# Kernel tuning notes

Hardware: AMD Instinct MI355X
Metric: run time of the kernel (lower is better)

## Reference

```python
import jax, jax.numpy as jnp
import numpy as np
from jax import lax

B, C_IN, T = 64, 16, 8192
HID, OUT = 64, 10
NEW_T = T // 4            # two MaxPool1d(2)
N_NODES = B * NEW_T       # 131072
N_EDGES = 2_097_152       # avg degree 16


def setup_inputs() -> dict:
    key = jax.random.key(0)
    ks = jax.random.split(key, 8)
    x = jax.random.normal(ks[0], (B, C_IN, T), dtype=jnp.float32)
    edge_index = jax.random.randint(ks[1], (2, N_EDGES), 0, N_NODES, dtype=jnp.int32)
    s = 0.05
    return {
        "x": x,
        "edge_index": edge_index,
        "conv1_w": jax.random.normal(ks[2], (16, C_IN, 5), dtype=jnp.float32) * s,
        "conv1_b": jnp.zeros((16,), jnp.float32),
        "conv2_w": jax.random.normal(ks[3], (32, 16, 5), dtype=jnp.float32) * s,
        "conv2_b": jnp.zeros((32,), jnp.float32),
        "gcn1_w": jax.random.normal(ks[4], (32, HID), dtype=jnp.float32) * s,
        "gcn1_b": jnp.zeros((HID,), jnp.float32),
        "gcn2_w": jax.random.normal(ks[5], (HID, HID), dtype=jnp.float32) * s,
        "gcn2_b": jnp.zeros((HID,), jnp.float32),
        "cls_w": jax.random.normal(ks[6], (HID, OUT), dtype=jnp.float32) * s,
        "cls_b": jnp.zeros((OUT,), jnp.float32),
    }


def conv1d(x, w, b):
    # x: [B, Cin, T], w: [Cout, Cin, K], padding=2 -> same length
    y = lax.conv_general_dilated(x, w, window_strides=(1,), padding=[(2, 2)],
                                 dimension_numbers=("NCH", "OIH", "NCH"))
    return y + b[None, :, None]


def maxpool2(x):
    # non-overlapping MaxPool1d(kernel=2) over last dim
    b, c, t = x.shape
    return x.reshape(b, c, t // 2, 2).max(axis=-1)


def gcn_conv(x, edge_index, W, b, n):
    # PyG GCNConv: add self-loops, symmetric normalization, scatter-add aggregate
    row, col = edge_index[0], edge_index[1]   # source j, target i
    loop = jnp.arange(n, dtype=row.dtype)
    row = jnp.concatenate([row, loop])
    col = jnp.concatenate([col, loop])
    deg = jax.ops.segment_sum(jnp.ones(row.shape, x.dtype), col, num_segments=n)
    dis = jnp.where(deg > 0, lax.rsqrt(deg), jnp.zeros_like(deg))
    norm = dis[row] * dis[col]                # [E+N]
    xw = x @ W                                # [N, out]
    msg = xw[row] * norm[:, None]             # gather along edges
    out = jax.ops.segment_sum(msg, col, num_segments=n)
    return out + b


def reference(x, edge_index, conv1_w, conv1_b, conv2_w, conv2_b,
              gcn1_w, gcn1_b, gcn2_w, gcn2_b, cls_w, cls_b):
    h = maxpool2(jax.nn.relu(conv1d(x, conv1_w, conv1_b)))     # [B,16,T/2]
    h = maxpool2(jax.nn.relu(conv1d(h, conv2_w, conv2_b)))     # [B,32,T/4]
    feat = h.transpose(0, 2, 1).reshape(-1, 32)                # [B*new_T, 32]
    n = feat.shape[0]
    g = jax.nn.relu(gcn_conv(feat, edge_index, gcn1_w, gcn1_b, n))
    g = jax.nn.relu(gcn_conv(g, edge_index, gcn2_w, gcn2_b, n))
    pooled = g.reshape(B, -1, HID).mean(axis=1)                # [B, HID]
    return pooled @ cls_w + cls_b                               # [B, OUT]
```

## Files before the change

### kernel.cpp

```cpp
#include <hip/hip_runtime.h>
#include <hip/hip_bf16.h>
#include <hip/hip_fp16.h>

#define BATCH 64
#define C_IN 16
#define T0 8192
#define T1 4096
#define T2 2048
#define N_NODES (BATCH * T2)
#define HID 64
#define NOUT 10

#define NCB 256
#define CB_SHIFT 9
#define CB_TGT 512
#define RCAP 9216
#define PC_EDGES 2048
#define PC_CAP 28

#define PK_RMASK 0x1FFFF

#define EC 1024

#define ZROW N_NODES

#define ROWW 24

#define FP8_SCALE 256.0f
#define FP8_SINV  (1.0f / 256.0f)

typedef __fp16 half8 __attribute__((ext_vector_type(8)));
typedef __fp16 half4v __attribute__((ext_vector_type(4)));
typedef float floatx4 __attribute__((ext_vector_type(4)));
typedef float floatx2 __attribute__((ext_vector_type(2)));

__global__ __launch_bounds__(256) void conv1_partition(
    const float* __restrict__ x, const float* __restrict__ w,
    const float* __restrict__ bias, __fp16* __restrict__ h1,
    const int* __restrict__ ei, int E,
    int* __restrict__ rcnt, int* __restrict__ gpairs,
    float* __restrict__ pool, unsigned char* __restrict__ xw,
    unsigned char* __restrict__ xw2) {
  __shared__ int smem_i[NCB + NCB * PC_CAP];
  if ((blockIdx.x & 1) == 0) {
    __fp16* xs = (__fp16*)smem_i;
    int bid = blockIdx.x >> 1;
    int b = bid >> 4;
    int tp0 = (bid & 15) * 256;
    if (bid == 0) {
      for (int k = threadIdx.x; k < BATCH * HID; k += 256) pool[k] = 0.f;
      if (threadIdx.x < 16) {
        ((unsigned*)(xw + (size_t)ZROW * 64))[threadIdx.x] = 0u;
        ((unsigned*)(xw2 + (size_t)ZROW * 64))[threadIdx.x] = 0u;
      }
    }
    int t_base = 2 * tp0 - 8;
    const float* xb = x + (size_t)b * C_IN * T0;
    for (int idx = threadIdx.x; idx < 16 * 132; idx += 256) {
      int ci = idx & 15;
      int c4 = idx >> 4;
      int gt = t_base + c4 * 4;
      float4 v = make_float4(0.f, 0.f, 0.f, 0.f);
      if (gt >= 0 && gt + 4 <= T0) v = *(const float4*)(xb + ci * T0 + gt);
      __fp16* d = xs + (c4 * 4) * ROWW + ci;
      d[0] = (__fp16)v.x;
      d[ROWW] = (__fp16)v.y;
      d[2 * ROWW] = (__fp16)v.z;
      d[3 * ROWW] = (__fp16)v.w;
    }
    int ln = threadIdx.x & 15;
    int q = (threadIdx.x & 63) >> 4;
    int wib = threadIdx.x >> 6;
    half8 wb[3];
#pragma unroll
    for (int ks = 0; ks < 3; ++ks) {
      int kk = ks * 2 + (q >> 1);
#pragma unroll
      for (int j = 0; j < 8; ++j) {
        int ci = (q & 1) * 8 + j;
        float wv = (kk < 5) ? w[(ln * 16 + ci) * 5 + kk] : 0.f;
        wb[ks][j] = (__fp16)wv;
      }
    }
    float bv = bias[ln];
    __syncthreads();
    int qh = q >> 1, qo = (q & 1) * 8;
#pragma unroll 2
    for (int mtl = 0; mtl < 8; ++mtl) {
      int mt = wib * 8 + mtl;
      int posb = mt * 16 + ln + qh + 6;
      half8 a0 = *(const half8*)(xs + posb * ROWW + qo);
      half8 a1 = *(const half8*)(xs + (posb + 2) * ROWW + qo);
      half8 a2 = *(const half8*)(xs + (posb + 4) * ROWW + qo);
      floatx4 c0 = {0.f, 0.f, 0.f, 0.f};
      c0 = __builtin_amdgcn_mfma_f32_16x16x32_f16(a0, wb[0], c0, 0, 0, 0);
      c0 = __builtin_amdgcn_mfma_f32_16x16x32_f16(a1, wb[1], c0, 0, 0, 0);
      c0 = __builtin_amdgcn_mfma_f32_16x16x32_f16(a2, wb[2], c0, 0, 0, 0);
      int tp = tp0 + mt * 8 + q * 2;
      size_t o = ((size_t)b * T1 + tp) * 16 + ln;
      h1[o] = (__fp16)fmaxf(fmaxf(c0[0], c0[1]) + bv, 0.f);
      h1[o + 16] = (__fp16)fmaxf(fmaxf(c0[2], c0[3]) + bv, 0.f);
    }
  } else {
    int* lcnt = smem_i;
    int* lpk = smem_i + NCB;
    int pid = blockIdx.x >> 1;
    if (threadIdx.x < NCB) lcnt[threadIdx.x] = 0;
    __syncthreads();
    int e0 = pid * PC_EDGES;
#pragma unroll
    for (int j = 0; j < PC_EDGES / 256; ++j) {
      int e = e0 + j * 256 + threadIdx.x;
      if (e < E) {
        int r = ei[e];
        int c = ei[E + e];
        int cb = c >> CB_SHIFT;
        int pk = r | ((c & (CB_TGT - 1)) << 17);
        int slot = atomicAdd(&lcnt[cb], 1);
        if (slot < PC_CAP) {
          lpk[cb * PC_CAP + slot] = pk;
        } else {
          int pos = atomicAdd(&rcnt[cb], 1);
          if (pos < RCAP) gpairs[(size_t)cb * RCAP + pos] = pk;
        }
      }
    }
    __syncthreads();
    int t = threadIdx.x;
    if (t < NCB) {
      int n = lcnt[t];
      if (n > PC_CAP) n = PC_CAP;
      if (n > 0) {
        int base = atomicAdd(&rcnt[t], n);
        int* dst = gpairs + (size_t)t * RCAP;
        for (int k = 0; k < n; ++k) {
          int p = base + k;
          if (p < RCAP) dst[p] = lpk[t * PC_CAP + k];
        }
      }
    }
  }
}

__global__ __launch_bounds__(256) void conv2_gemm1(const __fp16* __restrict__ h1,
    const float* __restrict__ w, const float* __restrict__ bias,
    const float* __restrict__ W1, const float* __restrict__ dis,
    unsigned char* __restrict__ xw) {
  __shared__ __fp16 xs[520 * ROWW];
  __shared__ __fp16 fs[256 * 40];
  int b = blockIdx.x >> 3;
  int tp0 = (blockIdx.x & 7) * 256;
  int t_base = 2 * tp0 - 2;
  for (int idx = threadIdx.x; idx < 520 * 2; idx += 256) {
    int row = idx >> 1;
    int hf = idx & 1;
    int gt = t_base + row;
    half8 v;
#pragma unroll
    for (int j = 0; j < 8; ++j) v[j] = (__fp16)0.f;
    if (gt >= 0 && gt < T1) v = *(const half8*)(h1 + ((size_t)b * T1 + gt) * 16 + hf * 8);
    *(half8*)(xs + row * ROWW + hf * 8) = v;
  }
  int ln = threadIdx.x & 15;
  int q = (threadIdx.x & 63) >> 4;
  int wib = threadIdx.x >> 6;
  half8 wb[2][3];
#pragma unroll
  for (int nt = 0; nt < 2; ++nt)
#pragma unroll
    for (int ks = 0; ks < 3; ++ks) {
      int kk = ks * 2 + (q >> 1);
#pragma unroll
      for (int j = 0; j < 8; ++j) {
        int ci = (q & 1) * 8 + j;
        float wv = (kk < 5) ? w[((nt * 16 + ln) * 16 + ci) * 5 + kk] : 0.f;
        wb[nt][ks][j] = (__fp16)wv;
      }
    }
  float b20 = bias[ln];
  float b21 = bias[16 + ln];
  __syncthreads();
  int qh = q >> 1, qo = (q & 1) * 8;
#pragma unroll 2
  for (int mtl = 0; mtl < 8; ++mtl) {
    int mt = wib * 8 + mtl;
    int posb = mt * 16 + ln + qh;
    half8 a0 = *(const half8*)(xs + posb * ROWW + qo);
    half8 a1 = *(const half8*)(xs + (posb + 2) * ROWW + qo);
    half8 a2 = *(const half8*)(xs + (posb + 4) * ROWW + qo);
    floatx4 c0 = {0.f, 0.f, 0.f, 0.f};
    floatx4 c1 = {0.f, 0.f, 0.f, 0.f};
    c0 = __builtin_amdgcn_mfma_f32_16x16x32_f16(a0, wb[0][0], c0, 0, 0, 0);
    c0 = __builtin_amdgcn_mfma_f32_16x16x32_f16(a1, wb[0][1], c0, 0, 0, 0);
    c0 = __builtin_amdgcn_mfma_f32_16x16x32_f16(a2, wb[0][2], c0, 0, 0, 0);
    c1 = __builtin_amdgcn_mfma_f32_16x16x32_f16(a0, wb[1][0], c1, 0, 0, 0);
    c1 = __builtin_amdgcn_mfma_f32_16x16x32_f16(a1, wb[1][1], c1, 0, 0, 0);
    c1 = __builtin_amdgcn_mfma_f32_16x16x32_f16(a2, wb[1][2], c1, 0, 0, 0);
    int node = wib * 64 + mtl * 8 + q * 2;
    fs[node * 40 + ln] = (__fp16)fmaxf(fmaxf(c0[0], c0[1]) + b20, 0.f);
    fs[(node + 1) * 40 + ln] = (__fp16)fmaxf(fmaxf(c0[2], c0[3]) + b20, 0.f);
    fs[node * 40 + 16 + ln] = (__fp16)fmaxf(fmaxf(c1[0], c1[1]) + b21, 0.f);
    fs[(node + 1) * 40 + 16 + ln] = (__fp16)fmaxf(fmaxf(c1[2], c1[3]) + b21, 0.f);
  }
  half8 bf[4];
#pragma unroll
  for (int t = 0; t < 4; ++t)
#pragma unroll
    for (int j = 0; j < 8; ++j)
      bf[t][j] = (__fp16)W1[(q * 8 + j) * 64 + ln * 4 + t];
  int gnode0 = b * T2 + tp0;
#pragma unroll
  for (int tt = 0; tt < 4; ++tt) {
    int lbase = (wib * 4 + tt) * 16;
    half8 a = *(const half8*)(fs + (lbase + ln) * 40 + q * 8);
    float d[4];
#pragma unroll
    for (int r = 0; r < 4; ++r) d[r] = dis[gnode0 + lbase + q * 4 + r] * FP8_SCALE;
    floatx4 acc[4];
#pragma unroll
    for (int t = 0; t < 4; ++t) {
      floatx4 z = {0.f, 0.f, 0.f, 0.f};
      acc[t] = __builtin_amdgcn_mfma_f32_16x16x32_f16(a, bf[t], z, 0, 0, 0);
    }
#pragma unroll
    for (int r = 0; r < 4; ++r) {
      int u = __builtin_amdgcn_cvt_pk_fp8_f32(acc[0][r] * d[r], acc[1][r] * d[r], 0, 0);
      u = __builtin_amdgcn_cvt_pk_fp8_f32(acc[2][r] * d[r], acc[3][r] * d[r], u, 1);
      *(unsigned*)(xw + (size_t)(gnode0 + lbase + q * 4 + r) * 64 + ln * 4) = (unsigned)u;
    }
  }
}

__global__ __launch_bounds__(512) void build_csr(const int* __restrict__ gpairs,
    const int* __restrict__ rcnt, int* __restrict__ ebuf,
    int* __restrict__ estart, int* __restrict__ ecnt, float* __restrict__ dis) {
  __shared__ int deg[CB_TGT];
  __shared__ int cur[CB_TGT];
  __shared__ int sc[CB_TGT];
  __shared__ int wsum[8];
  int b = blockIdx.x;
  int t = threadIdx.x;
  deg[t] = 0;
  cur[t] = 0;
  __syncthreads();
  int m = rcnt[b];
  if (m > RCAP) m = RCAP;
  const int* reg = gpairs + (size_t)b * RCAP;
  for (int k = t; k < m; k += 512)
    atomicAdd(&deg[(reg[k] >> 17) & (CB_TGT - 1)], 1);
  __syncthreads();
  int d = deg[t];
  int lane = t & 63;
  int wv = t >> 6;
  int sum = d;
#pragma unroll
  for (int off = 1; off < 64; off <<= 1) {
    int v = __shfl_up(sum, off, 64);
    if (lane >= off) sum += v;
  }
  if (lane == 63) wsum[wv] = sum;
  __syncthreads();
  int prefix = 0;
#pragma unroll
  for (int i = 0; i < 8; ++i) prefix += (i < wv) ? wsum[i] : 0;
  int excl = prefix + sum - d;
  int gi = (b << CB_SHIFT) + t;
  int base = b * RCAP;
  estart[gi] = base + excl;
  ecnt[gi] = d;
  dis[gi] = rsqrtf((float)d + 1.0f);
  sc[t] = excl;
  __syncthreads();
  for (int k = t; k < m; k += 512) {
    int p = reg[k];
    int lc = (p >> 17) & (CB_TGT - 1);
    int off = atomicAdd(&cur[lc], 1);
    ebuf[base + sc[lc] + off] = p & PK_RMASK;
  }
}

#define LOADW(dst_, b0_)                                                        \
  _Pragma("unroll")                                                             \
  for (int j = 0; j < 4; ++j) {                                                 \
    unsigned r = (unsigned)sidx[(b0_) + j * 4];                                 \
    dst_[j] = *(const unsigned*)(tab + ((r << 6) + ch4));                       \
  }
#define LOADWT(dst_, stl_, s0_, c_)                                             \
  _Pragma("unroll")                                                             \
  for (int j = 0; j < 4; ++j) {                                                 \
    int k = (s0_) + j * 4 + es;                                                 \
    unsigned r = (unsigned)sidx[(stl_) + k];                                    \
    unsigned off = (k < (c_)) ? ((r << 6) + ch4) : zoff;                        \
    dst_[j] = *(const unsigned*)(tab + off);                                    \
  }
#define CONSW(src_, ALO, AHI)                                                   \
  _Pragma("unroll")                                                             \
  for (int j = 0; j < 4; ++j) {                                                 \
    ALO += __builtin_amdgcn_cvt_pk_f32_fp8(src_[j], 0);                         \
    AHI += __builtin_amdgcn_cvt_pk_f32_fp8(src_[j], 1);                         \
  }
#define GATHER_NODE(c_, stl_, ALO, AHI)                                         \
  {                                                                             \
    int sb_ = (stl_) + es;                                                      \
    int nt_ = ((c_) + 15) >> 4;                                                 \
    int nf_ = (c_) >> 4;                                                        \
    unsigned wa_[4], wb_[4];                                                    \
    if (nt_ > 0) {                                                              \
      if (nf_ > 0) { LOADW(wa_, sb_) } else { LOADWT(wa_, stl_, 0, c_) }        \
    }                                                                           \
    for (int w_ = 0; w_ < nt_; ++w_) {                                          \
      int n_ = w_ + 1;                                                          \
      if (n_ < nt_) {                                                           \
        if (w_ & 1) {                                                           \
          if (n_ < nf_) { LOADW(wa_, sb_ + (n_ << 4)) }                         \
          else { LOADWT(wa_, stl_, n_ << 4, c_) }                               \
        } else {                                                                \
          if (n_ < nf_) { LOADW(wb_, sb_ + (n_ << 4)) }                         \
          else { LOADWT(wb_, stl_, n_ << 4, c_) }                               \
        }                                                                       \
      }                                                                         \
      if (w_ & 1) { CONSW(wb_, ALO, AHI) } else { CONSW(wa_, ALO, AHI) }        \
    }                                                                           \
  }

__global__ __launch_bounds__(256) void agg1_gemm2(const unsigned char* __restrict__ tab,
    const int* __restrict__ ebuf, const int* __restrict__ estart,
    const int* __restrict__ ecnt, const float* __restrict__ dis,
    const float* __restrict__ bias, const float* __restrict__ W2,
    unsigned char* __restrict__ xw2, int N) {
  __shared__ __fp16 g1s[16 * 72];
  __shared__ int sidx[EC + 16];
  __shared__ int sst[16], scn[16];
  int t = threadIdx.x;
  int base16 = blockIdx.x * 16;
  if (t < 16) {
    sst[t] = estart[base16 + t];
    scn[t] = ecnt[base16 + t];
  }
  __syncthreads();
  int span0 = sst[0];
  int total = sst[15] + scn[15] - span0;
  if (total > EC) total = EC;
  for (int k = t; k < total; k += 256) sidx[k] = ebuf[span0 + k];
  __syncthreads();
  int lane = t & 63;
  int es = lane >> 4;
  int ch = lane & 15;
  int wib = t >> 6;
  unsigned ch4 = (unsigned)ch * 4u;
  unsigned zoff = ((unsigned)ZROW << 6) + ch4;
  float4 bv = *(const float4*)(bias + ch * 4);
  half8 b0, b1;
#pragma unroll
  for (int j = 0; j < 8; ++j) {
    b0[j] = (__fp16)W2[((lane >> 4) * 8 + j) * 64 + wib * 16 + (lane & 15)];
    b1[j] = (__fp16)W2[(32 + (lane >> 4) * 8 + j) * 64 + wib * 16 + (lane & 15)];
  }
  unsigned swv[4];
#pragma unroll
  for (int jj = 0; jj < 4; ++jj)
    swv[jj] = *(const unsigned*)(tab + (((unsigned)(base16 + wib * 4 + jj) << 6) + ch4));
#pragma unroll
  for (int jj = 0; jj < 4; ++jj) {
    int il = wib * 4 + jj;
    int i = base16 + il;
    int stl = sst[il] - span0;
    int c = scn[il];
    if (stl + c > EC) c = (EC > stl) ? (EC - stl) : 0;
    float di = dis[i] * FP8_SINV;
    floatx2 aLO = {0.f, 0.f}, aHI = {0.f, 0.f};
    GATHER_NODE(c, stl, aLO, aHI)
    float ax = aLO.x, ay = aLO.y, az = aHI.x, aw = aHI.y;
    ax += __shfl_xor(ax, 16, 64); ax += __shfl_xor(ax, 32, 64);
    ay += __shfl_xor(ay, 16, 64); ay += __shfl_xor(ay, 32, 64);
    az += __shfl_xor(az, 16, 64); az += __shfl_xor(az, 32, 64);
    aw += __shfl_xor(aw, 16, 64); aw += __shfl_xor(aw, 32, 64);
    floatx2 slo = __builtin_amdgcn_cvt_pk_f32_fp8(swv[jj], 0);
    floatx2 shi = __builtin_amdgcn_cvt_pk_f32_fp8(swv[jj], 1);
    if (es == 0) {
      half4v r;
      r[0] = (__fp16)fmaxf((ax + slo.x) * di + bv.x, 0.f);
      r[1] = (__fp16)fmaxf((ay + slo.y) * di + bv.y, 0.f);
      r[2] = (__fp16)fmaxf((az + shi.x) * di + bv.z, 0.f);
      r[3] = (__fp16)fmaxf((aw + shi.y) * di + bv.w, 0.f);
      *(half4v*)(g1s + il * 72 + ch * 4) = r;
    }
  }
  __syncthreads();
  int m = lane & 15;
  int q = lane >> 4;
  half8 a0 = *(const half8*)(g1s + m * 72 + q * 8);
  half8 a1 = *(const half8*)(g1s + m * 72 + 32 + q * 8);
  floatx4 acc = {0.f, 0.f, 0.f, 0.f};
  acc = __builtin_amdgcn_mfma_f32_16x16x32_f16(a0, b0, acc, 0, 0, 0);
  acc = __builtin_amdgcn_mfma_f32_16x16x32_f16(a1, b1, acc, 0, 0, 0);
  float sv[4];
#pragma unroll
  for (int r = 0; r < 4; ++r)
    sv[r] = acc[r] * dis[base16 + q * 4 + r] * FP8_SCALE;
  int u = __builtin_amdgcn_cvt_pk_fp8_f32(sv[0], sv[1], 0, 0);
  u = __builtin_amdgcn_cvt_pk_fp8_f32(sv[2], sv[3], u, 1);
#pragma unroll
  for (int r = 0; r < 4; ++r) {
    int node = base16 + q * 4 + r;
    xw2[(size_t)node * 64 + wib * 16 + m] = (unsigned char)(((unsigned)u) >> (8 * r));
  }
}

__global__ __launch_bounds__(256) void gcn_aggregate_pool(const unsigned char* __restrict__ tab,
    const int* __restrict__ ebuf, const int* __restrict__ estart,
    const int* __restrict__ ecnt, const float* __restrict__ dis,
    const float* __restrict__ bias, float* __restrict__ pool, int N) {
  __shared__ float4 red[4][16];
  __shared__ int sidx[EC + 16];
  __shared__ int sst[16], scn[16];
  int t = threadIdx.x;
  int base16 = blockIdx.x * 16;
  if (t < 16) {
    sst[t] = estart[base16 + t];
    scn[t] = ecnt[base16 + t];
  }
  __syncthreads();
  int span0 = sst[0];
  int total = sst[15] + scn[15] - span0;
  if (total > EC) total = EC;
  for (int k = t; k < total; k += 256) sidx[k] = ebuf[span0 + k];
  __syncthreads();
  int lane = t & 63;
  int es = lane >> 4;
  int ch = lane & 15;
  int wib = t >> 6;
  unsigned ch4 = (unsigned)ch * 4u;
  unsigned zoff = ((unsigned)ZROW << 6) + ch4;
  float4 bv = *(const float4*)(bias + ch * 4);
  unsigned swv[4];
#pragma unroll
  for (int jj = 0; jj < 4; ++jj)
    swv[jj] = *(const unsigned*)(tab + (((unsigned)(base16 + wib * 4 + jj) << 6) + ch4));
  float px = 0.f, py = 0.f, pz = 0.f, pw = 0.f;
#pragma unroll
  for (int jj = 0; jj < 4; ++jj) {
    int il = wib * 4 + jj;
    int i = base16 + il;
    int stl = sst[il] - span0;
    int c = scn[il];
    if (stl + c > EC) c = (EC > stl) ? (EC - stl) : 0;
    float di = dis[i] * FP8_SINV;
    floatx2 aLO = {0.f, 0.f}, aHI = {0.f, 0.f};
    GATHER_NODE(c, stl, aLO, aHI)
    float ax = aLO.x, ay = aLO.y, az = aHI.x, aw = aHI.y;
    ax += __shfl_xor(ax, 16, 64); ax += __shfl_xor(ax, 32, 64);
    ay += __shfl_xor(ay, 16, 64); ay += __shfl_xor(ay, 32, 64);
    az += __shfl_xor(az, 16, 64); az += __shfl_xor(az, 32, 64);
    aw += __shfl_xor(aw, 16, 64); aw += __shfl_xor(aw, 32, 64);
    floatx2 slo = __builtin_amdgcn_cvt_pk_f32_fp8(swv[jj], 0);
    floatx2 shi = __builtin_amdgcn_cvt_pk_f32_fp8(swv[jj], 1);
    px += fmaxf((ax + slo.x) * di + bv.x, 0.f);
    py += fmaxf((ay + slo.y) * di + bv.y, 0.f);
    pz += fmaxf((az + shi.x) * di + bv.z, 0.f);
    pw += fmaxf((aw + shi.y) * di + bv.w, 0.f);
  }
  if (es == 0) red[wib][ch] = make_float4(px, py, pz, pw);
  __syncthreads();
  if (threadIdx.x < 64) {
    int f = threadIdx.x;
    int c4 = f >> 2, j4 = f & 3;
    const float* r0 = (const float*)&red[0][c4];
    const float* r1 = (const float*)&red[1][c4];
    const float* r2 = (const float*)&red[2][c4];
    const float* r3 = (const float*)&red[3][c4];
    float sum = r0[j4] + r1[j4] + r2[j4] + r3[j4];
    int b = (blockIdx.x * 16) >> 11;
    atomicAdd(&pool[b * 64 + f], sum);
  }
}

__global__ __launch_bounds__(64) void classify(const float* __restrict__ pool,
    const float* __restrict__ cw, const float* __restrict__ cb,
    float* __restrict__ out) {
  __shared__ float pl[64];
  int b = blockIdx.x;
  int t = threadIdx.x;
  pl[t] = pool[b * 64 + t] * (1.0f / (float)T2);
  __syncthreads();
  if (t < NOUT) {
    float a = cb[t];
#pragma unroll
    for (int k = 0; k < 64; ++k) a += pl[k] * cw[k * NOUT + t];
    out[b * NOUT + t] = a;
  }
}

extern "C" void kernel_launch(void* const* d_in, const int* in_sizes, int n_in,
                              void* d_out, int out_size, void* d_ws, size_t ws_size,
                              hipStream_t stream) {
  const float* x    = (const float*)d_in[0];
  const int*   ei   = (const int*)d_in[1];
  const float* c1w  = (const float*)d_in[2];
  const float* c1b  = (const float*)d_in[3];
  const float* c2w  = (const float*)d_in[4];
  const float* c2b  = (const float*)d_in[5];
  const float* g1w  = (const float*)d_in[6];
  const float* g1b  = (const float*)d_in[7];
  const float* g2w  = (const float*)d_in[8];
  const float* g2b  = (const float*)d_in[9];
  const float* cw   = (const float*)d_in[10];
  const float* cb   = (const float*)d_in[11];
  float* out = (float*)d_out;
  int E = in_sizes[1] / 2;
  const int N = N_NODES;

  char* ws = (char*)d_ws;
  int*    gpairs = (int*)(ws);
  int*    ebuf   = (int*)(ws + 9437184);
  int*    rcnt   = (int*)(ws + 18874368);
  int*    estart = (int*)(ws + 18878464);
  int*    ecnt   = (int*)(ws + 19402752);
  float*  dis    = (float*)(ws + 19927040);
  float*  pool   = (float*)(ws + 20451328);
  unsigned char* xw  = (unsigned char*)(ws + 20467712);
  unsigned char* xw2 = (unsigned char*)(ws + 37245184);
  __fp16* h1     = (__fp16*)(ws + 54022656);

  hipMemsetAsync(rcnt, 0, NCB * sizeof(int), stream);

  conv1_partition<<<dim3(BATCH * 16 * 2), dim3(256), 0, stream>>>(
      x, c1w, c1b, h1, ei, E, rcnt, gpairs, pool, xw, xw2);

  build_csr<<<dim3(NCB), dim3(512), 0, stream>>>(gpairs, rcnt, ebuf, estart, ecnt, dis);

  conv2_gemm1<<<dim3(BATCH * 8), dim3(256), 0, stream>>>(h1, c2w, c2b, g1w, dis, xw);
  agg1_gemm2<<<dim3(N / 16), dim3(256), 0, stream>>>(xw, ebuf, estart, ecnt, dis, g1b, g2w, xw2, N);
  gcn_aggregate_pool<<<dim3(N / 16), dim3(256), 0, stream>>>(xw2, ebuf, estart, ecnt, dis, g2b, pool, N);

  classify<<<dim3(BATCH), dim3(64), 0, stream>>>(pool, cw, cb, out);
}
```

Before: 247.6 us.

## Replace atomic bucket partition with histogram, scan, and deterministic scatter passes

The edge partition into column buckets used to rely on shared-memory slots plus global atomics on per-bucket counters. It now runs as three passes: a per-block histogram fused with conv1, a per-bucket prefix scan across blocks, and a scatter that writes each edge to a precomputed offset. This removes contention on the global counters and the overflow path, at the cost of two extra kernel launches and reading the edge array twice. The CSR build loop is also unrolled 4x so its loads can be in flight together.

```diff
diff --git a/kernel.cpp b/kernel.cpp
--- a/kernel.cpp
+++ b/kernel.cpp
@@ -16,7 +16,7 @@
 #define CB_TGT 512
 #define RCAP 9216
 #define PC_EDGES 2048
-#define PC_CAP 28
+#define NPB 1024
 
 #define PK_RMASK 0x1FFFF
 
@@ -34,16 +34,28 @@
 typedef float floatx4 __attribute__((ext_vector_type(4)));
 typedef float floatx2 __attribute__((ext_vector_type(2)));
 
-__global__ __launch_bounds__(256) void conv1_partition(
+__global__ __launch_bounds__(256) void conv1_hist(
     const float* __restrict__ x, const float* __restrict__ w,
     const float* __restrict__ bias, __fp16* __restrict__ h1,
-    const int* __restrict__ ei, int E,
-    int* __restrict__ rcnt, int* __restrict__ gpairs,
+    const int* __restrict__ ei, int E, int* __restrict__ hist,
     float* __restrict__ pool, unsigned char* __restrict__ xw,
     unsigned char* __restrict__ xw2) {
-  __shared__ int smem_i[NCB + NCB * PC_CAP];
-  if ((blockIdx.x & 1) == 0) {
-    __fp16* xs = (__fp16*)smem_i;
+  __shared__ __fp16 xs[528 * ROWW];
+  __shared__ int lhist[NCB];
+  if (blockIdx.x & 1) {
+    int pid = blockIdx.x >> 1;
+    if (threadIdx.x < NCB) lhist[threadIdx.x] = 0;
+    __syncthreads();
+    int e0 = pid * PC_EDGES;
+    const int* col = ei + E;
+#pragma unroll
+    for (int j = 0; j < PC_EDGES / 256; ++j) {
+      int e = e0 + j * 256 + threadIdx.x;
+      if (e < E) atomicAdd(&lhist[col[e] >> CB_SHIFT], 1);
+    }
+    __syncthreads();
+    if (threadIdx.x < NCB) hist[pid * NCB + threadIdx.x] = lhist[threadIdx.x];
+  } else {
     int bid = blockIdx.x >> 1;
     int b = bid >> 4;
     int tp0 = (bid & 15) * 256;
@@ -101,43 +113,63 @@
       h1[o] = (__fp16)fmaxf(fmaxf(c0[0], c0[1]) + bv, 0.f);
       h1[o + 16] = (__fp16)fmaxf(fmaxf(c0[2], c0[3]) + bv, 0.f);
     }
-  } else {
-    int* lcnt = smem_i;
-    int* lpk = smem_i + NCB;
-    int pid = blockIdx.x >> 1;
-    if (threadIdx.x < NCB) lcnt[threadIdx.x] = 0;
-    __syncthreads();
-    int e0 = pid * PC_EDGES;
-#pragma unroll
-    for (int j = 0; j < PC_EDGES / 256; ++j) {
-      int e = e0 + j * 256 + threadIdx.x;
-      if (e < E) {
-        int r = ei[e];
-        int c = ei[E + e];
-        int cb = c >> CB_SHIFT;
-        int pk = r | ((c & (CB_TGT - 1)) << 17);
-        int slot = atomicAdd(&lcnt[cb], 1);
-        if (slot < PC_CAP) {
-          lpk[cb * PC_CAP + slot] = pk;
-        } else {
-          int pos = atomicAdd(&rcnt[cb], 1);
-          if (pos < RCAP) gpairs[(size_t)cb * RCAP + pos] = pk;
-        }
-      }
-    }
-    __syncthreads();
-    int t = threadIdx.x;
-    if (t < NCB) {
-      int n = lcnt[t];
-      if (n > PC_CAP) n = PC_CAP;
-      if (n > 0) {
-        int base = atomicAdd(&rcnt[t], n);
-        int* dst = gpairs + (size_t)t * RCAP;
-        for (int k = 0; k < n; ++k) {
-          int p = base + k;
-          if (p < RCAP) dst[p] = lpk[t * PC_CAP + k];
-        }
-      }
+  }
+}
+
+__global__ __launch_bounds__(256) void scan_hist(const int* __restrict__ hist,
+    int* __restrict__ base, int* __restrict__ rcnt) {
+  __shared__ int wsum[4];
+  int cb = blockIdx.x;
+  int t = threadIdx.x;
+  int v[4];
+#pragma unroll
+  for (int k = 0; k < 4; ++k) v[k] = hist[(t * 4 + k) * NCB + cb];
+  int s = v[0] + v[1] + v[2] + v[3];
+  int lane = t & 63;
+  int wv = t >> 6;
+  int incl = s;
+#pragma unroll
+  for (int off = 1; off < 64; off <<= 1) {
+    int u = __shfl_up(incl, off, 64);
+    if (lane >= off) incl += u;
+  }
+  if (lane == 63) wsum[wv] = incl;
+  __syncthreads();
+  int prefix = 0;
+#pragma unroll
+  for (int i = 0; i < 4; ++i) prefix += (i < wv) ? wsum[i] : 0;
+  int excl = prefix + incl - s;
+  int b0 = cb * RCAP;
+#pragma unroll
+  for (int k = 0; k < 4; ++k) {
+    base[(t * 4 + k) * NCB + cb] = b0 + excl;
+    excl += v[k];
+  }
+  if (t == 0) rcnt[cb] = wsum[0] + wsum[1] + wsum[2] + wsum[3];
+}
+
+__global__ __launch_bounds__(256) void scatter_pairs(const int* __restrict__ ei,
+    int E, const int* __restrict__ base, int* __restrict__ gpairs) {
+  __shared__ int cur[NCB];
+  int pid = blockIdx.x;
+  int t = threadIdx.x;
+  if (t < NCB) cur[t] = base[pid * NCB + t];
+  __syncthreads();
+  int e0 = pid * PC_EDGES;
+  int rr[8], cc[8];
+#pragma unroll
+  for (int j = 0; j < 8; ++j) {
+    int e = e0 + j * 256 + t;
+    rr[j] = (e < E) ? ei[e] : 0;
+    cc[j] = (e < E) ? ei[E + e] : -1;
+  }
+#pragma unroll
+  for (int j = 0; j < 8; ++j) {
+    if (cc[j] >= 0) {
+      int cb = cc[j] >> CB_SHIFT;
+      int slot = atomicAdd(&cur[cb], 1);
+      int pk = rr[j] | ((cc[j] & (CB_TGT - 1)) << 17);
+      if (slot < NCB * RCAP) gpairs[slot] = pk;
     }
   }
 }
@@ -271,11 +303,22 @@
   dis[gi] = rsqrtf((float)d + 1.0f);
   sc[t] = excl;
   __syncthreads();
-  for (int k = t; k < m; k += 512) {
-    int p = reg[k];
-    int lc = (p >> 17) & (CB_TGT - 1);
-    int off = atomicAdd(&cur[lc], 1);
-    ebuf[base + sc[lc] + off] = p & PK_RMASK;
+  for (int k0 = 0; k0 < m; k0 += 2048) {
+    int p[4], have[4];
+#pragma unroll
+    for (int u = 0; u < 4; ++u) {
+      int k = k0 + u * 512 + t;
+      have[u] = (k < m);
+      p[u] = have[u] ? reg[k] : 0;
+    }
+#pragma unroll
+    for (int u = 0; u < 4; ++u) {
+      if (have[u]) {
+        int lc = (p[u] >> 17) & (CB_TGT - 1);
+        int off = atomicAdd(&cur[lc], 1);
+        ebuf[base + sc[lc] + off] = p[u] & PK_RMASK;
+      }
+    }
   }
 }
 
@@ -513,6 +556,8 @@
   char* ws = (char*)d_ws;
   int*    gpairs = (int*)(ws);
   int*    ebuf   = (int*)(ws + 9437184);
+  int*    hist   = ebuf;
+  int*    base   = (int*)(ws + 9437184 + 1048576);
   int*    rcnt   = (int*)(ws + 18874368);
   int*    estart = (int*)(ws + 18878464);
   int*    ecnt   = (int*)(ws + 19402752);
@@ -522,11 +567,11 @@
   unsigned char* xw2 = (unsigned char*)(ws + 37245184);
   __fp16* h1     = (__fp16*)(ws + 54022656);
 
-  hipMemsetAsync(rcnt, 0, NCB * sizeof(int), stream);
-
-  conv1_partition<<<dim3(BATCH * 16 * 2), dim3(256), 0, stream>>>(
-      x, c1w, c1b, h1, ei, E, rcnt, gpairs, pool, xw, xw2);
-
+
+  conv1_hist<<<dim3(BATCH * 16 * 2), dim3(256), 0, stream>>>(
+      x, c1w, c1b, h1, ei, E, hist, pool, xw, xw2);
+  scan_hist<<<dim3(NCB), dim3(256), 0, stream>>>(hist, base, rcnt);
+  scatter_pairs<<<dim3(NPB), dim3(256), 0, stream>>>(ei, E, base, gpairs);
   build_csr<<<dim3(NCB), dim3(512), 0, stream>>>(gpairs, rcnt, ebuf, estart, ecnt, dis);
 
   conv2_gemm1<<<dim3(BATCH * 8), dim3(256), 0, stream>>>(h1, c2w, c2b, g1w, dis, xw);
```

Result: slower. 261.5 us (+5.6%).
